# Performance work log

Hardware: AMD Instinct MI355X
Metric: run time of the kernel (lower is better)

Reference implementation:

```python
import jax, jax.numpy as jnp
import numpy as np

A0 = 0.529177249
SIGMA = jnp.array([0.5515909, 1.8886297, 1.3225029, 1.2316629,
                   2.1884933, 1.7750372, 1.3677907, 1.3820058], dtype=jnp.float32)


def celu(x):
    return jax.nn.celu(x, alpha=0.1)


def setup_inputs() -> dict:
    key = jax.random.key(0)
    ks = jax.random.split(key, 24)
    N, n, L, E = 512, 64, 384, 8
    H1, H2, H3 = 160, 128, 96
    s = 0.05
    f32 = jnp.float32
    return {
        "species": jax.random.randint(ks[0], (N, n), 0, E, dtype=jnp.int32),
        "coordinates": 3.0 * jax.random.normal(ks[1], (N, n, 3), dtype=f32),
        "net_charge": jax.random.normal(ks[2], (N,), dtype=f32),
        "aev": jax.random.normal(ks[3], (N, n, L), dtype=f32),
        "chi_W1": s * jax.random.normal(ks[4], (L, H1), dtype=f32),
        "chi_b1": s * jax.random.normal(ks[5], (H1,), dtype=f32),
        "chi_W2": s * jax.random.normal(ks[6], (H1, H2), dtype=f32),
        "chi_b2": s * jax.random.normal(ks[7], (H2,), dtype=f32),
        "chi_W3": s * jax.random.normal(ks[8], (H2, H3), dtype=f32),
        "chi_b3": s * jax.random.normal(ks[9], (H3,), dtype=f32),
        "chi_W4": s * jax.random.normal(ks[10], (H3, 1), dtype=f32),
        "chi_b4": s * jax.random.normal(ks[11], (1,), dtype=f32),
        "W1": s * jax.random.normal(ks[12], (E, L + 2, H1), dtype=f32),
        "b1": s * jax.random.normal(ks[13], (E, H1), dtype=f32),
        "W2": s * jax.random.normal(ks[14], (E, H1, H2), dtype=f32),
        "b2": s * jax.random.normal(ks[15], (E, H2), dtype=f32),
        "W3": s * jax.random.normal(ks[16], (E, H2, H3), dtype=f32),
        "b3": s * jax.random.normal(ks[17], (E, H3), dtype=f32),
        "W4": s * jax.random.normal(ks[18], (E, H3), dtype=f32),
        "b4": s * jax.random.normal(ks[19], (E,), dtype=f32),
    }


def _forward(species, coordinates, net_charge, aev,
             chi_W1, chi_b1, chi_W2, chi_b2, chi_W3, chi_b3, chi_W4, chi_b4,
             W1, b1, W2, b2, W3, b3, W4, b4):
    N, n = species.shape
    aev_flat = aev.reshape(N * n, -1)                       # (A, L)

    # nonzero_batch_dmat: distances in atomic units, eps avoids div-by-zero
    diff = coordinates[:, None, :, :] - coordinates[:, :, None, :]
    dist = jnp.sqrt(jnp.sum(diff * diff, -1) + 1e-16) / A0   # (N, n, n)

    pad = (species != -1).astype(aev.dtype)                  # (N, n)
    pair_mask = pad[:, None, :] * pad[:, :, None]            # (N, n, n)
    num_atoms = pad.sum(axis=1)                              # (N,)
    valid = (species.reshape(-1) != -1)                      # (A,)

    # chi_net: 4-layer MLP (CELU 0.1) + Softplus, masked to valid atoms
    h = celu(aev_flat @ chi_W1 + chi_b1)
    h = celu(h @ chi_W2 + chi_b2)
    h = celu(h @ chi_W3 + chi_b3)
    chi = jax.nn.softplus(h @ chi_W4 + chi_b4)[:, 0]
    chi = jnp.where(valid, chi, 0.0).reshape(N, n)

    chi_sum = chi.sum(axis=-1)
    k_net = 1.0 + jnp.abs(net_charge) / chi_sum
    chi_mean = chi_sum / num_atoms
    k_p = jnp.where(net_charge > 0, k_net, 1.0)
    k_n = jnp.where(net_charge < 0, k_net, 1.0)
    q = (-k_n[:, None] * chi + (k_p * chi_mean)[:, None]) * pad  # (N, n)

    # ESPerf: pairwise erf-screened Coulomb potential
    sig = SIGMA[jnp.clip(species, 0)]                        # (N, n)
    sig_sqsum = sig[:, None, :] ** 2 + sig[:, :, None] ** 2
    sig_sqsum = jnp.maximum(sig_sqsum, 1e-8)
    j_ij = jax.scipy.special.erf(dist / jnp.sqrt(2.0 * sig_sqsum)) / dist
    diag_mask = 1.0 - jnp.eye(n, dtype=dist.dtype)
    esp = (q[:, :, None] * j_ij * pair_mask * diag_mask[None]).sum(axis=-2)  # (N, n)
    coulomb_energy = 0.5 * (q * esp).sum(axis=-1)            # (N,)

    # species-routed expert MLPs over [aev | charge | esp] features
    feat = jnp.concatenate(
        [aev_flat, q.reshape(-1, 1), esp.reshape(-1, 1)], axis=1)  # (A, L+2)
    h1 = celu(jnp.einsum('ad,edh->aeh', feat, W1) + b1)      # (A, E, H1)
    h2 = celu(jnp.einsum('aeh,ehk->aek', h1, W2) + b2)       # (A, E, H2)
    h3 = celu(jnp.einsum('aek,ekm->aem', h2, W3) + b3)       # (A, E, H3)
    out_all = jnp.einsum('aem,em->ae', h3, W4) + b4          # (A, E)

    sp = jnp.clip(species.reshape(-1), 0)
    out = jnp.take_along_axis(out_all, sp[:, None], axis=1)[:, 0]
    out = jnp.where(valid, out, 0.0).reshape(N, n)
    mol_energy = out.sum(axis=1)
    return species, mol_energy + coulomb_energy, q


def reference(species, coordinates, net_charge, aev,
              chi_W1, chi_b1, chi_W2, chi_b2, chi_W3, chi_b3, chi_W4, chi_b4,
              W1, b1, W2, b2, W3, b3, W4, b4):
    return _forward(species, coordinates, net_charge, aev,
                    chi_W1, chi_b1, chi_W2, chi_b2, chi_W3, chi_b3, chi_W4, chi_b4,
                    W1, b1, W2, b2, W3, b3, W4, b4)
```

## Files before the change

### kernel.cpp

```cpp
#include <hip/hip_runtime.h>
#include <math.h>

#define A0_INV (1.0f/0.529177249f)

typedef __bf16 bf16x8 __attribute__((ext_vector_type(8)));
typedef __bf16 bf16x4 __attribute__((ext_vector_type(4)));
typedef float  f32x4  __attribute__((ext_vector_type(4)));

__device__ __constant__ float c_SIGMA[8] = {
    0.5515909f, 1.8886297f, 1.3225029f, 1.2316629f,
    2.1884933f, 1.7750372f, 1.3677907f, 1.3820058f};

__device__ __forceinline__ float celu01(float x) {
    return x > 0.0f ? x : 0.1f * (__expf(x * 10.0f) - 1.0f);
}
__device__ __forceinline__ float softplusf_(float x) {
    return fmaxf(x, 0.0f) + log1pf(__expf(-fabsf(x)));
}
__device__ __forceinline__ __bf16 u16_to_bf16(unsigned short u) {
    __bf16 b; __builtin_memcpy(&b, &u, 2); return b;
}
__device__ __forceinline__ unsigned short f_to_bf16_bits(float f) {
    __bf16 b = (__bf16)f; unsigned short u; __builtin_memcpy(&u, &b, 2); return u;
}

__device__ __forceinline__ void pack_one(int idx, const float* __restrict__ W,
                                         __bf16* __restrict__ Bp,
                                         int K, int OUT, int NT, int KT)
{
    int lane = idx & 63;
    int rest = idx >> 6;
    int kt = rest % KT; rest /= KT;
    int nt = rest % NT;
    int e  = rest / NT;
    int col = nt * 16 + (lane & 15);
    int k0  = kt * 32 + (lane >> 4) * 8;
    bf16x8 o;
#pragma unroll
    for (int j = 0; j < 8; ++j) {
        int k = k0 + j;
        float v = (k < K) ? W[((long)e * K + k) * OUT + col] : 0.0f;
        o[j] = (__bf16)v;
    }
    *((bf16x8*)Bp + idx) = o;
}

__global__ __launch_bounds__(256) void pack_all_kernel(
    const float* __restrict__ cW1, const float* __restrict__ cW2, const float* __restrict__ cW3,
    const float* __restrict__ W1,  const float* __restrict__ W2,  const float* __restrict__ W3,
    __bf16* bp_c1, __bf16* bp_c2, __bf16* bp_c3,
    __bf16* bp_e1, __bf16* bp_e2, __bf16* bp_e3)
{
    int idx = blockIdx.x * 256 + threadIdx.x;
    if      (idx <   7680) pack_one(idx,          cW1, bp_c1, 384, 160, 10, 12);
    else if (idx <  10240) pack_one(idx - 7680,   cW2, bp_c2, 160, 128,  8,  5);
    else if (idx <  11776) pack_one(idx - 10240,  cW3, bp_c3, 128,  96,  6,  4);
    else if (idx <  78336) pack_one(idx - 11776,  W1,  bp_e1, 386, 160, 10, 13);
    else if (idx <  98816) pack_one(idx - 78336,  W2,  bp_e2, 160, 128,  8,  5);
    else if (idx < 111104) pack_one(idx - 98816,  W3,  bp_e3, 128,  96,  6,  4);
}

template<int NT, int KT, int INS, int OUTS, bool CELU>
__device__ __forceinline__ void mlp_layer8(const __bf16* sIn, const bf16x8* __restrict__ Bp,
                                           const float* __restrict__ bias, __bf16* sOut, int tid)
{
    const int lane = tid & 63;
    const int wid  = tid >> 6;
    const int mw   = wid >> 2;
    const int nw   = wid & 3;
    const int r16  = lane & 15;
    const int g    = lane >> 4;
    constexpr int NJ = (NT + 3) / 4;
    f32x4 acc[2][NJ];
#pragma unroll
    for (int mi = 0; mi < 2; ++mi)
#pragma unroll
        for (int j = 0; j < NJ; ++j)
            acc[mi][j] = (f32x4){0.f, 0.f, 0.f, 0.f};

    bf16x8 b0[NJ], b1v[NJ];
#pragma unroll
    for (int j = 0; j < NJ; ++j) {
        const int nt = nw + 4 * j;
        if (nt < NT) {
            b0[j] = Bp[(nt * KT) * 64 + lane];
            if (KT > 1) b1v[j] = Bp[(nt * KT + 1) * 64 + lane];
        }
    }
    for (int kt = 0; kt < KT; ++kt) {
        bf16x8 a[2];
#pragma unroll
        for (int mi = 0; mi < 2; ++mi)
            a[mi] = *(const bf16x8*)(sIn + ((mw * 2 + mi) * 16 + r16) * INS + kt * 32 + g * 8);
        bf16x8 bn[NJ];
        if (kt + 2 < KT) {
#pragma unroll
            for (int j = 0; j < NJ; ++j) {
                const int nt = nw + 4 * j;
                if (nt < NT) bn[j] = Bp[(nt * KT + kt + 2) * 64 + lane];
            }
        }
#pragma unroll
        for (int j = 0; j < NJ; ++j) {
            const int nt = nw + 4 * j;
            if (nt < NT) {
#pragma unroll
                for (int mi = 0; mi < 2; ++mi)
                    acc[mi][j] = __builtin_amdgcn_mfma_f32_16x16x32_bf16(a[mi], b0[j], acc[mi][j], 0, 0, 0);
            }
        }
#pragma unroll
        for (int j = 0; j < NJ; ++j) { b0[j] = b1v[j]; b1v[j] = bn[j]; }
    }
#pragma unroll
    for (int j = 0; j < NJ; ++j) {
        const int nt = nw + 4 * j;
        if (nt < NT) {
            const float bb = bias[nt * 16 + r16];
#pragma unroll
            for (int mi = 0; mi < 2; ++mi)
#pragma unroll
                for (int r = 0; r < 4; ++r) {
                    float v = acc[mi][j][r] + bb;
                    if (CELU) v = celu01(v);
                    sOut[((mw * 2 + mi) * 16 + g * 4 + r) * OUTS + nt * 16 + r16] = (__bf16)v;
                }
        }
    }
}

__device__ __forceinline__ float l4_dot(const __bf16* __restrict__ h,
                                        const float* __restrict__ w4)
{
    float acc = 0.f;
#pragma unroll
    for (int u8 = 0; u8 < 12; ++u8) {
        bf16x8 hv = *(const bf16x8*)(h + u8 * 8);
        float4 wa = *(const float4*)(w4 + u8 * 8);
        float4 wb = *(const float4*)(w4 + u8 * 8 + 4);
        acc = fmaf((float)hv[0], wa.x, acc);
        acc = fmaf((float)hv[1], wa.y, acc);
        acc = fmaf((float)hv[2], wa.z, acc);
        acc = fmaf((float)hv[3], wa.w, acc);
        acc = fmaf((float)hv[4], wb.x, acc);
        acc = fmaf((float)hv[5], wb.y, acc);
        acc = fmaf((float)hv[6], wb.z, acc);
        acc = fmaf((float)hv[7], wb.w, acc);
    }
    return acc;
}

__global__ __launch_bounds__(512) void chimol_kernel(
    const float* __restrict__ aev, const int* __restrict__ species,
    const float* __restrict__ coords, const float* __restrict__ netq,
    const __bf16* __restrict__ bp1, const __bf16* __restrict__ bp2, const __bf16* __restrict__ bp3,
    const float* __restrict__ b1, const float* __restrict__ b2, const float* __restrict__ b3,
    const float* __restrict__ W4, const float* __restrict__ b4,
    __bf16* __restrict__ aev16,
    int* __restrict__ blockCounts, int* __restrict__ rank,
    float* __restrict__ qv, float* __restrict__ esp, float* __restrict__ coul,
    float* __restrict__ o_species, float* __restrict__ o_q)
{
    __shared__ __align__(16) unsigned char smem[50176 + 21504];
    __shared__ float sChi[64];
    __shared__ float sx[64], sy[64], sz[64], sq[64], ss2[64];
    __shared__ float sEsp[8][64];
    __bf16* sFeat = (__bf16*)smem;
    __bf16* sAct1 = (__bf16*)(smem + 50176);
    __bf16* sAct2 = (__bf16*)smem;
    __bf16* sAct3 = (__bf16*)(smem + 17408);
    const int t = threadIdx.x;
    const int m = blockIdx.x;
    const long base = (long)m * 64;

    if (aev16) {
        for (int i = t; i < 64 * 96; i += 512) {
            int row = i / 96, c4 = (i - row * 96) * 4;
            float4 v = *(const float4*)(aev + (base + row) * 384 + c4);
            bf16x4 o = {(__bf16)v.x, (__bf16)v.y, (__bf16)v.z, (__bf16)v.w};
            *(bf16x4*)(sFeat + row * 392 + c4) = o;
            *(bf16x4*)(aev16 + (base + row) * 384 + c4) = o;
        }
    } else {
        for (int i = t; i < 64 * 96; i += 512) {
            int row = i / 96, c4 = (i - row * 96) * 4;
            float4 v = *(const float4*)(aev + (base + row) * 384 + c4);
            bf16x4 o = {(__bf16)v.x, (__bf16)v.y, (__bf16)v.z, (__bf16)v.w};
            *(bf16x4*)(sFeat + row * 392 + c4) = o;
        }
    }
    __syncthreads();
    mlp_layer8<10, 12, 392, 168, true>(sFeat, (const bf16x8*)bp1, b1, sAct1, t);
    __syncthreads();
    mlp_layer8<8, 5, 168, 136, true>(sAct1, (const bf16x8*)bp2, b2, sAct2, t);
    __syncthreads();
    mlp_layer8<6, 4, 136, 104, true>(sAct2, (const bf16x8*)bp3, b3, sAct3, t);
    __syncthreads();
    if (t < 64) {
        float acc = l4_dot(sAct3 + t * 104, W4);
        float chiv = softplusf_(acc + b4[0]);
        long atom = base + t;
        int s = species[atom];
        if (s == -1) chiv = 0.f;
        sChi[t] = chiv;
        unsigned long long mym = 0;
#pragma unroll
        for (int e = 0; e < 8; ++e) {
            unsigned long long bm = __ballot(s == e);
            if (t == e) blockCounts[m * 8 + e] = (int)__popcll(bm);
            if (s == e) mym = bm;
        }
        if (s >= 0) rank[atom] = (int)__popcll(mym & ((1ull << t) - 1ull));
    }
    __syncthreads();

    const int j = t & 63, grp = t >> 6;
    const int atom = (int)base + j;
    int s = species[atom];
    float pad = (s != -1) ? 1.0f : 0.0f;
    float chij = sChi[j];

    float cs = chij, na = pad;
#pragma unroll
    for (int o = 32; o > 0; o >>= 1) {
        cs += __shfl_xor(cs, o);
        na += __shfl_xor(na, o);
    }
    float qc = netq[m];
    float k_net = 1.0f + fabsf(qc) / cs;
    float chi_mean = cs / na;
    float k_p = (qc > 0.0f) ? k_net : 1.0f;
    float k_n = (qc < 0.0f) ? k_net : 1.0f;
    float qj = (-k_n * chij + k_p * chi_mean) * pad;

    float sg = c_SIGMA[s < 0 ? 0 : s];
    float x = coords[atom * 3 + 0], y = coords[atom * 3 + 1], z = coords[atom * 3 + 2];
    if (grp == 0) { sx[j] = x; sy[j] = y; sz[j] = z; sq[j] = qj; ss2[j] = sg * sg; }
    __syncthreads();

    float s2j = sg * sg;
    float ej = 0.0f;
#pragma unroll
    for (int k = 0; k < 8; ++k) {
        int i = grp * 8 + k;
        if (i == j) continue;
        float dx = sx[i] - x, dy = sy[i] - y, dz = sz[i] - z;
        float d = sqrtf(dx * dx + dy * dy + dz * dz + 1e-16f) * A0_INV;
        float ssum = fmaxf(ss2[i] + s2j, 1e-8f);
        float jij = erff(d * rsqrtf(2.0f * ssum)) / d;
        ej = fmaf(sq[i], jij, ej);
    }
    sEsp[grp][j] = ej;
    __syncthreads();
    if (grp == 0) {
        float e = ((sEsp[0][j] + sEsp[1][j]) + (sEsp[2][j] + sEsp[3][j]))
                + ((sEsp[4][j] + sEsp[5][j]) + (sEsp[6][j] + sEsp[7][j]));
        e *= pad;
        float ce = qj * e;
#pragma unroll
        for (int o = 32; o > 0; o >>= 1) ce += __shfl_xor(ce, o);
        if (j == 0) coul[m] = 0.5f * ce;
        qv[atom] = qj;
        esp[atom] = e;
        o_species[atom] = (float)s;
        o_q[atom] = qj;
    }
}

__global__ void bucket_scan_kernel(int* __restrict__ blockCounts,
                                   int* __restrict__ counts, int* __restrict__ offs,
                                   int* __restrict__ workItems, int* __restrict__ workCount,
                                   int nb)
{
    __shared__ int segSum[8][8];
    __shared__ int tot[8];
    const int tid = threadIdx.x;
    const int seg = tid >> 3, e = tid & 7;
    const int per = (nb + 7) / 8;
    const int b0 = seg * per, b1 = min(b0 + per, nb);
    int run = 0;
    for (int b = b0; b < b1; ++b) run += blockCounts[b * 8 + e];
    segSum[seg][e] = run;
    __syncthreads();
    if (tid < 8) {
        int r = 0;
        for (int s2 = 0; s2 < 8; ++s2) { int c = segSum[s2][tid]; segSum[s2][tid] = r; r += c; }
        tot[tid] = r;
    }
    __syncthreads();
    int runp = segSum[seg][e];
    for (int b = b0; b < b1; ++b) {
        int c = blockCounts[b * 8 + e];
        blockCounts[b * 8 + e] = runp;
        runp += c;
    }
    if (tid == 0) {
        int o = 0;
        for (int i = 0; i < 8; ++i) { offs[i] = o; counts[i] = tot[i]; o += tot[i]; }
        offs[8] = o;
    }
    if (tid < 8) {
        int pos = 0;
        for (int i = 0; i < tid; ++i) pos += (tot[i] + 63) >> 6;
        int nt_e = (tot[tid] + 63) >> 6;
        for (int k = 0; k < nt_e; ++k) workItems[pos + k] = (tid << 20) | (k * 64);
        if (tid == 7) workCount[0] = pos + nt_e;
    }
}

__global__ __launch_bounds__(256) void bucket_fill_kernel(
    const int* __restrict__ species, const int* __restrict__ blockCounts,
    const int* __restrict__ offs, const int* __restrict__ rank,
    int* __restrict__ bidx, float* __restrict__ outat, int A)
{
    int a = blockIdx.x * 256 + threadIdx.x;
    if (a < A) {
        outat[a] = 0.0f;
        int s = species[a];
        if (s >= 0)
            bidx[offs[s] + blockCounts[(a >> 6) * 8 + s] + rank[a]] = a;
    }
}

__device__ __forceinline__ bf16x8 loadA16(const __bf16* __restrict__ aev16,
                                          int atom, int kt, int g)
{
    bf16x8 z = {};
    if (atom < 0) return z;
    return *(const bf16x8*)(aev16 + (long)atom * 384 + kt * 32 + g * 8);
}
__device__ __forceinline__ bf16x8 loadAf(const float* __restrict__ aev,
                                         int atom, int kt, int g)
{
    bf16x8 z = {};
    if (atom < 0) return z;
    const float* p = aev + (long)atom * 384 + kt * 32 + g * 8;
    float4 va = *(const float4*)p, vb = *(const float4*)(p + 4);
    bf16x8 r = {(__bf16)va.x, (__bf16)va.y, (__bf16)va.z, (__bf16)va.w,
                (__bf16)vb.x, (__bf16)vb.y, (__bf16)vb.z, (__bf16)vb.w};
    return r;
}

template<bool HAVE16>
__global__ __launch_bounds__(512, 4) void expert_mfma_kernel(
    const float* __restrict__ aev, const __bf16* __restrict__ aev16,
    const float* __restrict__ qv, const float* __restrict__ esp,
    const __bf16* __restrict__ bp1, const __bf16* __restrict__ bp2, const __bf16* __restrict__ bp3,
    const float* __restrict__ b1, const float* __restrict__ b2, const float* __restrict__ b3,
    const float* __restrict__ W4, const float* __restrict__ b4,
    const int* __restrict__ counts, const int* __restrict__ offs, const int* __restrict__ bidx,
    const int* __restrict__ workItems, const int* __restrict__ workCount,
    float* __restrict__ outat)
{
    const int bid = blockIdx.x;
    if (bid >= workCount[0]) return;
    const int wi = workItems[bid];
    const int e = wi >> 20;
    const int start = wi & 0xFFFFF;
    const int cnt = counts[e];

    __shared__ __align__(16) unsigned char smem[21504 + 17408];
    __shared__ int said[64];
    __shared__ unsigned int sQE[64];
    __bf16* sAct1 = (__bf16*)smem;
    __bf16* sAct2 = (__bf16*)(smem + 21504);
    __bf16* sAct3 = (__bf16*)smem;
    const int t = threadIdx.x;

    if (t < 64) {
        int a_ = (start + t < cnt) ? bidx[offs[e] + start + t] : -1;
        said[t] = a_;
        float q = 0.f, es = 0.f;
        if (a_ >= 0) { q = qv[a_]; es = esp[a_]; }
        sQE[t] = ((unsigned)f_to_bf16_bits(es) << 16) | f_to_bf16_bits(q);
    }
    __syncthreads();

    {
        const int lane = t & 63, wid = t >> 6;
        const int mw = wid >> 2, nw = wid & 3;
        const int r16 = lane & 15, g = lane >> 4;
        const int atom0 = said[(mw * 2 + 0) * 16 + r16];
        const int atom1 = said[(mw * 2 + 1) * 16 + r16];
        const bf16x8* Bp = (const bf16x8*)bp1 + (size_t)e * 10 * 13 * 64;
        constexpr int NJ = 3;
        f32x4 acc[2][NJ];
#pragma unroll
        for (int mi = 0; mi < 2; ++mi)
#pragma unroll
            for (int j = 0; j < NJ; ++j) acc[mi][j] = (f32x4){0.f, 0.f, 0.f, 0.f};

        bf16x8 b0[NJ], b1v[NJ];
#pragma unroll
        for (int j = 0; j < NJ; ++j) {
            const int nt = nw + 4 * j;
            if (nt < 10) {
                b0[j]  = Bp[(nt * 13) * 64 + lane];
                b1v[j] = Bp[(nt * 13 + 1) * 64 + lane];
            }
        }
        bf16x8 a0c = HAVE16 ? loadA16(aev16, atom0, 0, g) : loadAf(aev, atom0, 0, g);
        bf16x8 a1c = HAVE16 ? loadA16(aev16, atom1, 0, g) : loadAf(aev, atom1, 0, g);

        for (int kt = 0; kt < 12; ++kt) {
            bf16x8 bn[NJ];
            if (kt + 2 < 13) {
#pragma unroll
                for (int j = 0; j < NJ; ++j) {
                    const int nt = nw + 4 * j;
                    if (nt < 10) bn[j] = Bp[(nt * 13 + kt + 2) * 64 + lane];
                }
            }
            bf16x8 a0n, a1n;
            if (kt < 11) {
                a0n = HAVE16 ? loadA16(aev16, atom0, kt + 1, g) : loadAf(aev, atom0, kt + 1, g);
                a1n = HAVE16 ? loadA16(aev16, atom1, kt + 1, g) : loadAf(aev, atom1, kt + 1, g);
            }
#pragma unroll
            for (int j = 0; j < NJ; ++j) {
                const int nt = nw + 4 * j;
                if (nt < 10) {
                    acc[0][j] = __builtin_amdgcn_mfma_f32_16x16x32_bf16(a0c, b0[j], acc[0][j], 0, 0, 0);
                    acc[1][j] = __builtin_amdgcn_mfma_f32_16x16x32_bf16(a1c, b0[j], acc[1][j], 0, 0, 0);
                }
            }
#pragma unroll
            for (int j = 0; j < NJ; ++j) { b0[j] = b1v[j]; b1v[j] = bn[j]; }
            if (kt < 11) { a0c = a0n; a1c = a1n; }
        }
        bf16x8 aq0 = {}, aq1 = {};
        if (g == 0) {
            unsigned qe0 = sQE[(mw * 2 + 0) * 16 + r16];
            unsigned qe1 = sQE[(mw * 2 + 1) * 16 + r16];
            aq0[0] = u16_to_bf16((unsigned short)(qe0 & 0xffff));
            aq0[1] = u16_to_bf16((unsigned short)(qe0 >> 16));
            aq1[0] = u16_to_bf16((unsigned short)(qe1 & 0xffff));
            aq1[1] = u16_to_bf16((unsigned short)(qe1 >> 16));
        }
#pragma unroll
        for (int j = 0; j < NJ; ++j) {
            const int nt = nw + 4 * j;
            if (nt < 10) {
                acc[0][j] = __builtin_amdgcn_mfma_f32_16x16x32_bf16(aq0, b0[j], acc[0][j], 0, 0, 0);
                acc[1][j] = __builtin_amdgcn_mfma_f32_16x16x32_bf16(aq1, b0[j], acc[1][j], 0, 0, 0);
            }
        }
#pragma unroll
        for (int j = 0; j < NJ; ++j) {
            const int nt = nw + 4 * j;
            if (nt < 10) {
                const float bb = b1[e * 160 + nt * 16 + r16];
#pragma unroll
                for (int mi = 0; mi < 2; ++mi)
#pragma unroll
                    for (int r = 0; r < 4; ++r) {
                        float v = acc[mi][j][r] + bb;
                        v = celu01(v);
                        sAct1[((mw * 2 + mi) * 16 + g * 4 + r) * 168 + nt * 16 + r16] = (__bf16)v;
                    }
            }
        }
    }
    __syncthreads();
    mlp_layer8<8, 5, 168, 136, true>(sAct1, (const bf16x8*)bp2 + (size_t)e * 8 * 5 * 64,
                                     b2 + e * 128, sAct2, t);
    __syncthreads();
    mlp_layer8<6, 4, 136, 104, true>(sAct2, (const bf16x8*)bp3 + (size_t)e * 6 * 4 * 64,
                                     b3 + e * 96, sAct3, t);
    __syncthreads();
    if (t < 64) {
        int atom = said[t];
        if (atom >= 0) {
            float acc = l4_dot(sAct3 + t * 104, W4 + e * 96);
            outat[atom] = acc + b4[e];
        }
    }
}

__global__ __launch_bounds__(64) void energy_kernel(
    const float* __restrict__ outat, const float* __restrict__ coul,
    float* __restrict__ o_energy)
{
    int m = blockIdx.x, t = threadIdx.x;
    float v = outat[m * 64 + t];
#pragma unroll
    for (int o = 32; o > 0; o >>= 1) v += __shfl_xor(v, o);
    if (t == 0) o_energy[m] = v + coul[m];
}

extern "C" void kernel_launch(void* const* d_in, const int* in_sizes, int n_in,
                              void* d_out, int out_size, void* d_ws, size_t ws_size,
                              hipStream_t stream)
{
    const int*   species = (const int*)  d_in[0];
    const float* coords  = (const float*)d_in[1];
    const float* netq    = (const float*)d_in[2];
    const float* aev     = (const float*)d_in[3];
    const float* cW1 = (const float*)d_in[4];
    const float* cb1 = (const float*)d_in[5];
    const float* cW2 = (const float*)d_in[6];
    const float* cb2 = (const float*)d_in[7];
    const float* cW3 = (const float*)d_in[8];
    const float* cb3 = (const float*)d_in[9];
    const float* cW4 = (const float*)d_in[10];
    const float* cb4 = (const float*)d_in[11];
    const float* W1  = (const float*)d_in[12];
    const float* b1  = (const float*)d_in[13];
    const float* W2  = (const float*)d_in[14];
    const float* b2  = (const float*)d_in[15];
    const float* W3  = (const float*)d_in[16];
    const float* b3  = (const float*)d_in[17];
    const float* W4  = (const float*)d_in[18];
    const float* b4  = (const float*)d_in[19];

    const int N = in_sizes[2];
    const int n = in_sizes[0] / N;
    const int A = N * n;
    const int nb64 = A / 64;
    const int maxWork = nb64 + 8;

    float* fbase   = (float*)d_ws;
    float* qv      = fbase;
    float* esp     = fbase + (size_t)A;
    float* outat   = fbase + (size_t)2 * A;
    float* coul    = fbase + (size_t)3 * A;
    int*   counts  = (int*)(coul + N);
    int*   offs    = counts + 8;
    int*   workCount = offs + 9;
    int*   workItems = workCount + 1;
    int*   blockCounts = workItems + maxWork;
    int*   rank    = blockCounts + nb64 * 8;
    int*   bidx    = rank + A;
    uintptr_t p = ((uintptr_t)(bidx + A) + 15) & ~(uintptr_t)15;
    __bf16* bp_c1 = (__bf16*)p; p += (size_t)10 * 12 * 512 * 2;
    __bf16* bp_c2 = (__bf16*)p; p += (size_t)8  * 5  * 512 * 2;
    __bf16* bp_c3 = (__bf16*)p; p += (size_t)6  * 4  * 512 * 2;
    __bf16* bp_e1 = (__bf16*)p; p += (size_t)8 * 10 * 13 * 512 * 2;
    __bf16* bp_e2 = (__bf16*)p; p += (size_t)8 * 8  * 5  * 512 * 2;
    __bf16* bp_e3 = (__bf16*)p; p += (size_t)8 * 6  * 4  * 512 * 2;
    p = (p + 15) & ~(uintptr_t)15;
    __bf16* aev16 = (__bf16*)p;
    size_t need = (p - (uintptr_t)d_ws) + (size_t)A * 384 * 2;
    if (ws_size < need) aev16 = nullptr;

    float* o_species = (float*)d_out;
    float* o_energy  = o_species + A;
    float* o_q       = o_energy + N;

    pack_all_kernel<<<(111104 + 255) / 256, 256, 0, stream>>>(
        cW1, cW2, cW3, W1, W2, W3, bp_c1, bp_c2, bp_c3, bp_e1, bp_e2, bp_e3);

    chimol_kernel<<<nb64, 512, 0, stream>>>(aev, species, coords, netq,
                                            bp_c1, bp_c2, bp_c3,
                                            cb1, cb2, cb3, cW4, cb4,
                                            aev16, blockCounts, rank,
                                            qv, esp, coul, o_species, o_q);
    bucket_scan_kernel<<<1, 64, 0, stream>>>(blockCounts, counts, offs,
                                             workItems, workCount, nb64);
    bucket_fill_kernel<<<(A + 255) / 256, 256, 0, stream>>>(species, blockCounts, offs,
                                                            rank, bidx, outat, A);
    if (aev16)
        expert_mfma_kernel<true><<<maxWork, 512, 0, stream>>>(
            aev, aev16, qv, esp, bp_e1, bp_e2, bp_e3, b1, b2, b3, W4, b4,
            counts, offs, bidx, workItems, workCount, outat);
    else
        expert_mfma_kernel<false><<<maxWork, 512, 0, stream>>>(
            aev, aev16, qv, esp, bp_e1, bp_e2, bp_e3, b1, b2, b3, W4, b4,
            counts, offs, bidx, workItems, workCount, outat);
    energy_kernel<<<N, 64, 0, stream>>>(outat, coul, o_energy);
}
```

Measured before the change: 95.33 us.

## Stage expert weights through double-buffered LDS and fuse bucket scan with fill

```diff
diff --git a/kernel.cpp b/kernel.cpp
--- a/kernel.cpp
+++ b/kernel.cpp
@@ -123,6 +123,73 @@
                 for (int r = 0; r < 4; ++r) {
                     float v = acc[mi][j][r] + bb;
                     if (CELU) v = celu01(v);
+                    sOut[((mw * 2 + mi) * 16 + g * 4 + r) * OUTS + nt * 16 + r16] = (__bf16)v;
+                }
+        }
+    }
+}
+
+template<int NT, int KT, int INS, int OUTS>
+__device__ __forceinline__ void mlp_ldsB(const __bf16* sIn, const __bf16* __restrict__ gB,
+                                         __bf16* Bbuf, const float* __restrict__ bias,
+                                         __bf16* sOut, int tid)
+{
+    const int lane = tid & 63;
+    const int wid  = tid >> 6;
+    const int mw   = wid >> 2;
+    const int nw   = wid & 3;
+    const int r16  = lane & 15;
+    const int g    = lane >> 4;
+    constexpr int NJ = (NT + 3) / 4;
+    constexpr int SL = NT * 512;
+    f32x4 acc[2][NJ];
+#pragma unroll
+    for (int mi = 0; mi < 2; ++mi)
+#pragma unroll
+        for (int j = 0; j < NJ; ++j)
+            acc[mi][j] = (f32x4){0.f, 0.f, 0.f, 0.f};
+
+    for (int f = wid; f < NT; f += 8)
+        *(bf16x8*)(Bbuf + f * 512 + lane * 8) =
+            *(const bf16x8*)(gB + ((size_t)f * KT) * 512 + lane * 8);
+    __syncthreads();
+
+    for (int kt = 0; kt < KT; ++kt) {
+        const int cur = kt & 1;
+        bf16x8 st0 = {}, st1 = {};
+        bool d0 = false, d1 = false;
+        if (kt + 1 < KT) {
+            if (wid < NT)     { st0 = *(const bf16x8*)(gB + ((size_t)wid * KT + kt + 1) * 512 + lane * 8); d0 = true; }
+            if (wid + 8 < NT) { st1 = *(const bf16x8*)(gB + ((size_t)(wid + 8) * KT + kt + 1) * 512 + lane * 8); d1 = true; }
+        }
+        bf16x8 a[2];
+#pragma unroll
+        for (int mi = 0; mi < 2; ++mi)
+            a[mi] = *(const bf16x8*)(sIn + ((mw * 2 + mi) * 16 + r16) * INS + kt * 32 + g * 8);
+#pragma unroll
+        for (int j = 0; j < NJ; ++j) {
+            const int nt = nw + 4 * j;
+            if (nt < NT) {
+                bf16x8 b = *(const bf16x8*)(Bbuf + cur * SL + nt * 512 + lane * 8);
+#pragma unroll
+                for (int mi = 0; mi < 2; ++mi)
+                    acc[mi][j] = __builtin_amdgcn_mfma_f32_16x16x32_bf16(a[mi], b, acc[mi][j], 0, 0, 0);
+            }
+        }
+        if (d0) *(bf16x8*)(Bbuf + (cur ^ 1) * SL + wid * 512 + lane * 8) = st0;
+        if (d1) *(bf16x8*)(Bbuf + (cur ^ 1) * SL + (wid + 8) * 512 + lane * 8) = st1;
+        __syncthreads();
+    }
+#pragma unroll
+    for (int j = 0; j < NJ; ++j) {
+        const int nt = nw + 4 * j;
+        if (nt < NT) {
+            const float bb = bias[nt * 16 + r16];
+#pragma unroll
+            for (int mi = 0; mi < 2; ++mi)
+#pragma unroll
+                for (int r = 0; r < 4; ++r) {
+                    float v = celu01(acc[mi][j][r] + bb);
                     sOut[((mw * 2 + mi) * 16 + g * 4 + r) * OUTS + nt * 16 + r16] = (__bf16)v;
                 }
         }
@@ -267,20 +334,24 @@
     }
 }
 
-__global__ void bucket_scan_kernel(int* __restrict__ blockCounts,
-                                   int* __restrict__ counts, int* __restrict__ offs,
-                                   int* __restrict__ workItems, int* __restrict__ workCount,
-                                   int nb)
+__global__ __launch_bounds__(1024) void scanfill_kernel(
+    const int* __restrict__ species, int* __restrict__ blockCounts,
+    int* __restrict__ counts, int* __restrict__ offs,
+    int* __restrict__ workItems, int* __restrict__ workCount,
+    const int* __restrict__ rank, int* __restrict__ bidx,
+    float* __restrict__ outat, int A, int nb)
 {
     __shared__ int segSum[8][8];
     __shared__ int tot[8];
     const int tid = threadIdx.x;
-    const int seg = tid >> 3, e = tid & 7;
     const int per = (nb + 7) / 8;
-    const int b0 = seg * per, b1 = min(b0 + per, nb);
-    int run = 0;
-    for (int b = b0; b < b1; ++b) run += blockCounts[b * 8 + e];
-    segSum[seg][e] = run;
+    if (tid < 64) {
+        const int seg = tid >> 3, e = tid & 7;
+        const int b0 = seg * per, b1 = min(b0 + per, nb);
+        int run = 0;
+        for (int b = b0; b < b1; ++b) run += blockCounts[b * 8 + e];
+        segSum[seg][e] = run;
+    }
     __syncthreads();
     if (tid < 8) {
         int r = 0;
@@ -288,11 +359,15 @@
         tot[tid] = r;
     }
     __syncthreads();
-    int runp = segSum[seg][e];
-    for (int b = b0; b < b1; ++b) {
-        int c = blockCounts[b * 8 + e];
-        blockCounts[b * 8 + e] = runp;
-        runp += c;
+    if (tid < 64) {
+        const int seg = tid >> 3, e = tid & 7;
+        const int b0 = seg * per, b1 = min(b0 + per, nb);
+        int runp = segSum[seg][e];
+        for (int b = b0; b < b1; ++b) {
+            int c = blockCounts[b * 8 + e];
+            blockCounts[b * 8 + e] = runp;
+            runp += c;
+        }
     }
     if (tid == 0) {
         int o = 0;
@@ -306,15 +381,8 @@
         for (int k = 0; k < nt_e; ++k) workItems[pos + k] = (tid << 20) | (k * 64);
         if (tid == 7) workCount[0] = pos + nt_e;
     }
-}
-
-__global__ __launch_bounds__(256) void bucket_fill_kernel(
-    const int* __restrict__ species, const int* __restrict__ blockCounts,
-    const int* __restrict__ offs, const int* __restrict__ rank,
-    int* __restrict__ bidx, float* __restrict__ outat, int A)
-{
-    int a = blockIdx.x * 256 + threadIdx.x;
-    if (a < A) {
+    __syncthreads();
+    for (int a = tid; a < A; a += 1024) {
         outat[a] = 0.0f;
         int s = species[a];
         if (s >= 0)
@@ -359,13 +427,17 @@
     const int start = wi & 0xFFFFF;
     const int cnt = counts[e];
 
-    __shared__ __align__(16) unsigned char smem[21504 + 17408];
+    __shared__ __align__(16) unsigned char smem[21504 + 17408 + 20480];
     __shared__ int said[64];
     __shared__ unsigned int sQE[64];
     __bf16* sAct1 = (__bf16*)smem;
     __bf16* sAct2 = (__bf16*)(smem + 21504);
     __bf16* sAct3 = (__bf16*)smem;
+    __bf16* Bbuf  = (__bf16*)(smem + 21504 + 17408);
     const int t = threadIdx.x;
+    const int lane = t & 63, wid = t >> 6;
+    const int mw = wid >> 2, nw = wid & 3;
+    const int r16 = lane & 15, g = lane >> 4;
 
     if (t < 64) {
         int a_ = (start + t < cnt) ? bidx[offs[e] + start + t] : -1;
@@ -377,73 +449,63 @@
     __syncthreads();
 
     {
-        const int lane = t & 63, wid = t >> 6;
-        const int mw = wid >> 2, nw = wid & 3;
-        const int r16 = lane & 15, g = lane >> 4;
+        const __bf16* gB = bp1 + (size_t)e * 10 * 13 * 512;
         const int atom0 = said[(mw * 2 + 0) * 16 + r16];
         const int atom1 = said[(mw * 2 + 1) * 16 + r16];
-        const bf16x8* Bp = (const bf16x8*)bp1 + (size_t)e * 10 * 13 * 64;
         constexpr int NJ = 3;
+        constexpr int SL = 10 * 512;
         f32x4 acc[2][NJ];
 #pragma unroll
         for (int mi = 0; mi < 2; ++mi)
 #pragma unroll
             for (int j = 0; j < NJ; ++j) acc[mi][j] = (f32x4){0.f, 0.f, 0.f, 0.f};
 
-        bf16x8 b0[NJ], b1v[NJ];
-#pragma unroll
-        for (int j = 0; j < NJ; ++j) {
-            const int nt = nw + 4 * j;
-            if (nt < 10) {
-                b0[j]  = Bp[(nt * 13) * 64 + lane];
-                b1v[j] = Bp[(nt * 13 + 1) * 64 + lane];
-            }
-        }
+        for (int f = wid; f < 10; f += 8)
+            *(bf16x8*)(Bbuf + f * 512 + lane * 8) =
+                *(const bf16x8*)(gB + ((size_t)f * 13) * 512 + lane * 8);
         bf16x8 a0c = HAVE16 ? loadA16(aev16, atom0, 0, g) : loadAf(aev, atom0, 0, g);
         bf16x8 a1c = HAVE16 ? loadA16(aev16, atom1, 0, g) : loadAf(aev, atom1, 0, g);
-
-        for (int kt = 0; kt < 12; ++kt) {
-            bf16x8 bn[NJ];
-            if (kt + 2 < 13) {
-#pragma unroll
-                for (int j = 0; j < NJ; ++j) {
-                    const int nt = nw + 4 * j;
-                    if (nt < 10) bn[j] = Bp[(nt * 13 + kt + 2) * 64 + lane];
-                }
+        __syncthreads();
+
+        for (int kt = 0; kt < 13; ++kt) {
+            const int cur = kt & 1;
+            bf16x8 st0 = {}, st1 = {};
+            bool d0 = false, d1 = false;
+            if (kt + 1 < 13) {
+                st0 = *(const bf16x8*)(gB + ((size_t)wid * 13 + kt + 1) * 512 + lane * 8); d0 = true;
+                if (wid + 8 < 10) { st1 = *(const bf16x8*)(gB + ((size_t)(wid + 8) * 13 + kt + 1) * 512 + lane * 8); d1 = true; }
             }
             bf16x8 a0n, a1n;
-            if (kt < 11) {
+            if (kt + 1 < 12) {
                 a0n = HAVE16 ? loadA16(aev16, atom0, kt + 1, g) : loadAf(aev, atom0, kt + 1, g);
                 a1n = HAVE16 ? loadA16(aev16, atom1, kt + 1, g) : loadAf(aev, atom1, kt + 1, g);
+            }
+            bf16x8 a0u = a0c, a1u = a1c;
+            if (kt == 12) {
+                bf16x8 z0 = {}, z1 = {};
+                if (g == 0) {
+                    unsigned qe0 = sQE[(mw * 2 + 0) * 16 + r16];
+                    unsigned qe1 = sQE[(mw * 2 + 1) * 16 + r16];
+                    z0[0] = u16_to_bf16((unsigned short)(qe0 & 0xffff));
+                    z0[1] = u16_to_bf16((unsigned short)(qe0 >> 16));
+                    z1[0] = u16_to_bf16((unsigned short)(qe1 & 0xffff));
+                    z1[1] = u16_to_bf16((unsigned short)(qe1 >> 16));
+                }
+                a0u = z0; a1u = z1;
             }
 #pragma unroll
             for (int j = 0; j < NJ; ++j) {
                 const int nt = nw + 4 * j;
                 if (nt < 10) {
-                    acc[0][j] = __builtin_amdgcn_mfma_f32_16x16x32_bf16(a0c, b0[j], acc[0][j], 0, 0, 0);
-                    acc[1][j] = __builtin_amdgcn_mfma_f32_16x16x32_bf16(a1c, b0[j], acc[1][j], 0, 0, 0);
+                    bf16x8 b = *(const bf16x8*)(Bbuf + cur * SL + nt * 512 + lane * 8);
+                    acc[0][j] = __builtin_amdgcn_mfma_f32_16x16x32_bf16(a0u, b, acc[0][j], 0, 0, 0);
+                    acc[1][j] = __builtin_amdgcn_mfma_f32_16x16x32_bf16(a1u, b, acc[1][j], 0, 0, 0);
                 }
             }
-#pragma unroll
-            for (int j = 0; j < NJ; ++j) { b0[j] = b1v[j]; b1v[j] = bn[j]; }
-            if (kt < 11) { a0c = a0n; a1c = a1n; }
-        }
-        bf16x8 aq0 = {}, aq1 = {};
-        if (g == 0) {
-            unsigned qe0 = sQE[(mw * 2 + 0) * 16 + r16];
-            unsigned qe1 = sQE[(mw * 2 + 1) * 16 + r16];
-            aq0[0] = u16_to_bf16((unsigned short)(qe0 & 0xffff));
-            aq0[1] = u16_to_bf16((unsigned short)(qe0 >> 16));
-            aq1[0] = u16_to_bf16((unsigned short)(qe1 & 0xffff));
-            aq1[1] = u16_to_bf16((unsigned short)(qe1 >> 16));
-        }
-#pragma unroll
-        for (int j = 0; j < NJ; ++j) {
-            const int nt = nw + 4 * j;
-            if (nt < 10) {
-                acc[0][j] = __builtin_amdgcn_mfma_f32_16x16x32_bf16(aq0, b0[j], acc[0][j], 0, 0, 0);
-                acc[1][j] = __builtin_amdgcn_mfma_f32_16x16x32_bf16(aq1, b0[j], acc[1][j], 0, 0, 0);
-            }
+            if (d0) *(bf16x8*)(Bbuf + (cur ^ 1) * SL + wid * 512 + lane * 8) = st0;
+            if (d1) *(bf16x8*)(Bbuf + (cur ^ 1) * SL + (wid + 8) * 512 + lane * 8) = st1;
+            __syncthreads();
+            if (kt + 1 < 12) { a0c = a0n; a1c = a1n; }
         }
 #pragma unroll
         for (int j = 0; j < NJ; ++j) {
@@ -454,19 +516,18 @@
                 for (int mi = 0; mi < 2; ++mi)
 #pragma unroll
                     for (int r = 0; r < 4; ++r) {
-                        float v = acc[mi][j][r] + bb;
-                        v = celu01(v);
+                        float v = celu01(acc[mi][j][r] + bb);
                         sAct1[((mw * 2 + mi) * 16 + g * 4 + r) * 168 + nt * 16 + r16] = (__bf16)v;
                     }
             }
         }
     }
     __syncthreads();
-    mlp_layer8<8, 5, 168, 136, true>(sAct1, (const bf16x8*)bp2 + (size_t)e * 8 * 5 * 64,
-                                     b2 + e * 128, sAct2, t);
-    __syncthreads();
-    mlp_layer8<6, 4, 136, 104, true>(sAct2, (const bf16x8*)bp3 + (size_t)e * 6 * 4 * 64,
-                                     b3 + e * 96, sAct3, t);
+    mlp_ldsB<8, 5, 168, 136>(sAct1, bp2 + (size_t)e * 8 * 5 * 512, Bbuf,
+                             b2 + e * 128, sAct2, t);
+    __syncthreads();
+    mlp_ldsB<6, 4, 136, 104>(sAct2, bp3 + (size_t)e * 6 * 4 * 512, Bbuf,
+                             b3 + e * 96, sAct3, t);
     __syncthreads();
     if (t < 64) {
         int atom = said[t];
@@ -555,10 +616,9 @@
                                             cb1, cb2, cb3, cW4, cb4,
                                             aev16, blockCounts, rank,
                                             qv, esp, coul, o_species, o_q);
-    bucket_scan_kernel<<<1, 64, 0, stream>>>(blockCounts, counts, offs,
-                                             workItems, workCount, nb64);
-    bucket_fill_kernel<<<(A + 255) / 256, 256, 0, stream>>>(species, blockCounts, offs,
-                                                            rank, bidx, outat, A);
+    scanfill_kernel<<<1, 1024, 0, stream>>>(species, blockCounts, counts, offs,
+                                            workItems, workCount, rank, bidx,
+                                            outat, A, nb64);
     if (aev16)
         expert_mfma_kernel<true><<<maxWork, 512, 0, stream>>>(
             aev, aev16, qv, esp, bp_e1, bp_e2, bp_e3, b1, b2, b3, W4, b4,
```

Result: slower. 121.4 us (+27.3%).
